# Kernel tuning notes

Hardware: AMD Instinct MI355X
Metric: run time of the kernel (lower is better)

The kernel has to match this reference:

```python
import jax, jax.numpy as jnp
import numpy as np

N_NODES = 50000
N_EDGES = 800000
N_RELS = 65
D = 64
N_GRAPHS = 512


def setup_inputs() -> dict:
    key = jax.random.key(0)
    ks = jax.random.split(key, 20)
    inp = {
        "node_feats": jax.random.normal(ks[0], (N_NODES, D), dtype=jnp.float32),
        "etypes": jax.random.randint(ks[1], (N_EDGES,), 0, N_RELS),
        "src": jax.random.randint(ks[2], (N_EDGES,), 0, N_NODES),
        "dst": jax.random.randint(ks[3], (N_EDGES,), 0, N_NODES),
        "graph_ids": jnp.sort(jax.random.randint(ks[4], (N_NODES,), 0, N_GRAPHS)),
    }
    s = 1.0 / np.sqrt(D)
    # 3 RGCN layers: per-relation weights (basis with num_bases=num_rels == full) + bias
    for i, k in zip(range(1, 4), (ks[5], ks[6], ks[7])):
        inp[f"W_rel{i}"] = jax.random.normal(k, (N_RELS, D, D), dtype=jnp.float32) * s
        inp[f"b{i}"] = jnp.zeros((D,), dtype=jnp.float32)
    # 3 FC layers
    for i, k in zip(range(1, 4), (ks[8], ks[9], ks[10])):
        inp[f"fc_W{i}"] = jax.random.normal(k, (D, D), dtype=jnp.float32) * s
        inp[f"fc_b{i}"] = jnp.zeros((D,), dtype=jnp.float32)
    inp["pred_W"] = jax.random.normal(ks[11], (D, 2), dtype=jnp.float32) * s
    inp["pred_b"] = jnp.zeros((2,), dtype=jnp.float32)
    return inp


def _rgcn_layer(h, W, b, etypes, src, dst):
    # all-relation projection: [N, R, K]
    proj = jnp.einsum('nd,rdk->nrk', h, W)
    # per-edge gather of relation-specific message: [E, K]
    msg = proj[src, etypes]
    # scatter-sum into destination nodes
    agg = jax.ops.segment_sum(msg, dst, num_segments=h.shape[0])
    return jax.nn.relu(agg + b)


def reference(node_feats, etypes, src, dst, graph_ids,
              W_rel1, b1, W_rel2, b2, W_rel3, b3,
              fc_W1, fc_b1, fc_W2, fc_b2, fc_W3, fc_b3,
              pred_W, pred_b):
    h = node_feats
    h = _rgcn_layer(h, W_rel1, b1, etypes, src, dst)
    h = _rgcn_layer(h, W_rel2, b2, etypes, src, dst)
    h = _rgcn_layer(h, W_rel3, b3, etypes, src, dst)
    # sum-pool nodes per graph: [G, D]
    g = jax.ops.segment_sum(h, graph_ids, num_segments=N_GRAPHS)
    g = jax.nn.relu(g @ fc_W1 + fc_b1)
    g = jax.nn.relu(g @ fc_W2 + fc_b2)
    g = jax.nn.relu(g @ fc_W3 + fc_b3)
    return g @ pred_W + pred_b
```

## Files before the change

kernel.cpp:

```cpp
#include <hip/hip_runtime.h>
#include <hip/hip_bf16.h>

#define N_NODES 50000
#define N_EDGES 800000
#define N_RELS 65
#define DIM 64
#define N_GRAPHS 512

#define SORT_BLOCKS 256
#define CHUNK ((N_EDGES + SORT_BLOCKS - 1) / SORT_BLOCKS)

#define SCAN_BLK 512
#define NSCAN_BLKS ((N_NODES + SCAN_BLK - 1) / SCAN_BLK)

#define MSG_BLOCKS 1024
#define NWAVES (MSG_BLOCKS * 4)

typedef __attribute__((ext_vector_type(8))) short short8;
typedef __attribute__((ext_vector_type(4))) float f32x4;


__global__ void conv_h_zero_kernel(const float* __restrict__ x, __hip_bfloat16* __restrict__ y,
                                   int* __restrict__ cnt_d, int* __restrict__ cnt_g) {
    int i = blockIdx.x * 256 + threadIdx.x;
    if (i < N_NODES * DIM) y[i] = __float2bfloat16(x[i]);
    if (i < N_NODES) cnt_d[i] = 0;
    if (i < N_GRAPHS) cnt_g[i] = 0;
}

__global__ void conv_wt3_kernel(const float* __restrict__ W1, const float* __restrict__ W2,
                                const float* __restrict__ W3,
                                __hip_bfloat16* __restrict__ Wt1,
                                __hip_bfloat16* __restrict__ Wt2,
                                __hip_bfloat16* __restrict__ Wt3) {
    const int n = N_RELS * DIM * DIM;
    int i = blockIdx.x * 256 + threadIdx.x;
    if (i >= 3 * n) return;
    int which = i / n, j = i - which * n;
    const float* W = (which == 0) ? W1 : (which == 1) ? W2 : W3;
    __hip_bfloat16* Wt = (which == 0) ? Wt1 : (which == 1) ? Wt2 : Wt3;
    int r = j >> 12, rest = j & 4095;
    int nn = rest >> 6, k = rest & 63;
    Wt[(size_t)r * 4096 + nn * 64 + k] = __float2bfloat16(W[(size_t)r * 4096 + k * 64 + nn]);
}


__global__ __launch_bounds__(256) void hist2_kernel(const int* __restrict__ et,
                                                    int* __restrict__ blk_hist) {
    __shared__ int lh[N_RELS];
    int t = threadIdx.x, b = blockIdx.x;
    if (t < N_RELS) lh[t] = 0;
    __syncthreads();
    int lo = b * CHUNK;
    int hi = lo + CHUNK; if (hi > N_EDGES) hi = N_EDGES;
    for (int i = lo + t; i < hi; i += 256) atomicAdd(&lh[et[i]], 1);
    __syncthreads();
    if (t < N_RELS) blk_hist[b * N_RELS + t] = lh[t];
}

__global__ __launch_bounds__(256) void relwave_kernel(const int* __restrict__ blk_hist,
                                                      int* __restrict__ blk_off,
                                                      int* __restrict__ rel_tot) {
    int wave = blockIdx.x * 4 + (threadIdx.x >> 6);
    int lane = threadIdx.x & 63;
    if (wave >= N_RELS) return;
    int run = 0;
    for (int c = 0; c < SORT_BLOCKS; c += 64) {
        int b = c + lane;
        int v = blk_hist[b * N_RELS + wave];
        int x = v;
        #pragma unroll
        for (int off = 1; off < 64; off <<= 1) {
            int y = __shfl_up(x, off);
            if (lane >= off) x += y;
        }
        blk_off[b * N_RELS + wave] = run + x - v;
        run += __shfl(x, 63);
    }
    if (lane == 0) rel_tot[wave] = run;
}

__global__ __launch_bounds__(128) void relbase_kernel(const int* __restrict__ rel_tot,
                                                      int* __restrict__ rel_ptr,
                                                      int* __restrict__ tile_base) {
    __shared__ int tot[N_RELS];
    int t = threadIdx.x;
    if (t < N_RELS) tot[t] = rel_tot[t];
    __syncthreads();
    if (t == 0) {
        int s = 0, tt = 0;
        for (int q = 0; q < N_RELS; ++q) {
            rel_ptr[q] = s; s += tot[q];
            tile_base[q] = tt; tt += (tot[q] + 15) >> 4;
        }
        rel_ptr[N_RELS] = N_EDGES;
        tile_base[N_RELS] = tt;
    }
}

__global__ __launch_bounds__(256) void scatter2_kernel(
    const int* __restrict__ et, const int* __restrict__ src,
    const int* __restrict__ dst, const int* __restrict__ blk_off,
    const int* __restrict__ rel_ptr,
    int* __restrict__ src_s, int* __restrict__ dst_s) {
    __shared__ int cur[N_RELS];
    int t = threadIdx.x, b = blockIdx.x;
    if (t < N_RELS) cur[t] = blk_off[b * N_RELS + t] + rel_ptr[t];
    __syncthreads();
    int lo = b * CHUNK;
    int hi = lo + CHUNK; if (hi > N_EDGES) hi = N_EDGES;
    for (int i = lo + t; i < hi; i += 256) {
        int r = et[i];
        int p = atomicAdd(&cur[r], 1);
        src_s[p] = src[i];
        dst_s[p] = dst[i];
    }
}


__global__ void histdst_kernel(const int* __restrict__ dst, int* __restrict__ cnt_d) {
    int i = blockIdx.x * 256 + threadIdx.x;
    if (i < N_EDGES) atomicAdd(&cnt_d[dst[i]], 1);
}

__global__ __launch_bounds__(SCAN_BLK) void scanblk_kernel(const int* __restrict__ cnt,
                                                           int* __restrict__ outv,
                                                           int* __restrict__ blk_tot) {
    __shared__ int tmp[SCAN_BLK];
    int t = threadIdx.x;
    int i = blockIdx.x * SCAN_BLK + t;
    int v = (i < N_NODES) ? cnt[i] : 0;
    tmp[t] = v;
    __syncthreads();
    for (int off = 1; off < SCAN_BLK; off <<= 1) {
        int add = (t >= off) ? tmp[t - off] : 0;
        __syncthreads();
        tmp[t] += add;
        __syncthreads();
    }
    if (i < N_NODES) outv[i] = tmp[t] - v;
    if (t == SCAN_BLK - 1) blk_tot[blockIdx.x] = tmp[t];
}

__global__ void scantop_kernel(int* __restrict__ blk_tot, int* __restrict__ blk_base) {
    if (threadIdx.x == 0 && blockIdx.x == 0) {
        int run = 0;
        for (int b = 0; b < NSCAN_BLKS; ++b) { blk_base[b] = run; run += blk_tot[b]; }
    }
}

__global__ __launch_bounds__(SCAN_BLK) void scanadd_kernel(int* __restrict__ outv,
                                                           int* __restrict__ cursor,
                                                           const int* __restrict__ blk_base) {
    int i = blockIdx.x * SCAN_BLK + threadIdx.x;
    if (i < N_NODES) {
        int v = outv[i] + blk_base[blockIdx.x];
        outv[i] = v;
        cursor[i] = v;
    }
}

__global__ void dpos_kernel(const int* __restrict__ dst_s, int* __restrict__ cursor,
                            int* __restrict__ dpos) {
    int i = blockIdx.x * 256 + threadIdx.x;
    if (i < N_EDGES) dpos[i] = atomicAdd(&cursor[dst_s[i]], 1);
}


__global__ void histgid_kernel(const int* __restrict__ gid, int* __restrict__ cnt_g) {
    int i = blockIdx.x * 256 + threadIdx.x;
    if (i < N_NODES) atomicAdd(&cnt_g[gid[i]], 1);
}

__global__ __launch_bounds__(512) void scangid_kernel(const int* __restrict__ cnt_g,
                                                      int* __restrict__ g_ptr) {
    __shared__ int tmp[512];
    int t = threadIdx.x;
    int v = (t < N_GRAPHS) ? cnt_g[t] : 0;
    tmp[t] = v;
    __syncthreads();
    for (int off = 1; off < 512; off <<= 1) {
        int add = (t >= off) ? tmp[t - off] : 0;
        __syncthreads();
        tmp[t] += add;
        __syncthreads();
    }
    if (t < N_GRAPHS) g_ptr[t] = tmp[t] - v;
}


__global__ __launch_bounds__(256) void msg_mfma_kernel(
    const __hip_bfloat16* __restrict__ hb, const __hip_bfloat16* __restrict__ Wt,
    const int* __restrict__ rel_ptr, const int* __restrict__ tile_base,
    const int* __restrict__ src_s, const int* __restrict__ dpos,
    __hip_bfloat16* __restrict__ msg) {
    __shared__ __align__(16) unsigned short stA[4][16 * 72];
    __shared__ __align__(16) float stC[4][16 * 68];

    int t = threadIdx.x;
    int w = t >> 6, lane = t & 63;
    int quad = lane >> 4, m16 = lane & 15;
    int wave = blockIdx.x * 4 + w;

    int ntiles = tile_base[N_RELS];
    int tpw = (ntiles + NWAVES - 1) / NWAVES;
    int T = wave * tpw;
    int T1 = T + tpw; if (T1 > ntiles) T1 = ntiles;
    if (T >= T1) return;

    unsigned short* sa = &stA[w][0];
    float* sc = &stC[w][0];

    int r = 0;
    while (T >= tile_base[r + 1]) ++r;

    while (T < T1) {
        int chunk_end = tile_base[r + 1]; if (chunk_end > T1) chunk_end = T1;
        int e_base = rel_ptr[r], t_base = tile_base[r];
        int seg_end = rel_ptr[r + 1];

        const __hip_bfloat16* Wr = Wt + (size_t)r * (DIM * DIM);
        short8 bf00 = *(const short8*)(Wr + (0 * 16 + m16) * DIM + 0 * 32 + quad * 8);
        short8 bf01 = *(const short8*)(Wr + (1 * 16 + m16) * DIM + 0 * 32 + quad * 8);
        short8 bf02 = *(const short8*)(Wr + (2 * 16 + m16) * DIM + 0 * 32 + quad * 8);
        short8 bf03 = *(const short8*)(Wr + (3 * 16 + m16) * DIM + 0 * 32 + quad * 8);
        short8 bf10 = *(const short8*)(Wr + (0 * 16 + m16) * DIM + 1 * 32 + quad * 8);
        short8 bf11 = *(const short8*)(Wr + (1 * 16 + m16) * DIM + 1 * 32 + quad * 8);
        short8 bf12 = *(const short8*)(Wr + (2 * 16 + m16) * DIM + 1 * 32 + quad * 8);
        short8 bf13 = *(const short8*)(Wr + (3 * 16 + m16) * DIM + 1 * 32 + quad * 8);

        auto eidx = [&](int TT) {
            int i = e_base + (TT - t_base) * 16 + lane;
            return i < N_EDGES ? i : N_EDGES - 1;
        };

        int sv_c, dp_c, sv_n = 0, dp_n = 0, sv_nn = 0, dp_nn = 0;
        uint4 g0_c, g1_c;
        {
            int i0 = eidx(T);
            sv_c = src_s[i0]; dp_c = dpos[i0];
            int r0 = lane >> 3;
            int s0 = __shfl(sv_c, r0);
            int s1 = __shfl(sv_c, r0 + 8);
            g0_c = *(const uint4*)(hb + (size_t)s0 * DIM + (lane & 7) * 8);
            g1_c = *(const uint4*)(hb + (size_t)s1 * DIM + (lane & 7) * 8);
            if (T + 1 < chunk_end) {
                int i1 = eidx(T + 1);
                sv_n = src_s[i1]; dp_n = dpos[i1];
            }
        }

        for (; T < chunk_end; ++T) {
            int e0 = e_base + (T - t_base) * 16;
            int rows = seg_end - e0; if (rows > 16) rows = 16;

            int r0 = lane >> 3;
            *(uint4*)&sa[r0 * 72 + (lane & 7) * 8] = g0_c;
            *(uint4*)&sa[(r0 + 8) * 72 + (lane & 7) * 8] = g1_c;

            uint4 g0_n, g1_n;
            bool hasN = (T + 1 < chunk_end);
            if (hasN) {
                int s0 = __shfl(sv_n, r0);
                int s1 = __shfl(sv_n, r0 + 8);
                g0_n = *(const uint4*)(hb + (size_t)s0 * DIM + (lane & 7) * 8);
                g1_n = *(const uint4*)(hb + (size_t)s1 * DIM + (lane & 7) * 8);
            }
            if (T + 2 < chunk_end) {
                int i2 = eidx(T + 2);
                sv_nn = src_s[i2]; dp_nn = dpos[i2];
            }

            short8 a0 = *(const short8*)&sa[m16 * 72 + quad * 8];
            short8 a1 = *(const short8*)&sa[m16 * 72 + 32 + quad * 8];

            f32x4 c0 = {0.f, 0.f, 0.f, 0.f}, c1 = c0, c2 = c0, c3 = c0;
            c0 = __builtin_amdgcn_mfma_f32_16x16x32_bf16(a0, bf00, c0, 0, 0, 0);
            c1 = __builtin_amdgcn_mfma_f32_16x16x32_bf16(a0, bf01, c1, 0, 0, 0);
            c2 = __builtin_amdgcn_mfma_f32_16x16x32_bf16(a0, bf02, c2, 0, 0, 0);
            c3 = __builtin_amdgcn_mfma_f32_16x16x32_bf16(a0, bf03, c3, 0, 0, 0);
            c0 = __builtin_amdgcn_mfma_f32_16x16x32_bf16(a1, bf10, c0, 0, 0, 0);
            c1 = __builtin_amdgcn_mfma_f32_16x16x32_bf16(a1, bf11, c1, 0, 0, 0);
            c2 = __builtin_amdgcn_mfma_f32_16x16x32_bf16(a1, bf12, c2, 0, 0, 0);
            c3 = __builtin_amdgcn_mfma_f32_16x16x32_bf16(a1, bf13, c3, 0, 0, 0);

            #pragma unroll
            for (int reg = 0; reg < 4; ++reg) {
                int rr = (quad * 4 + reg) * 68 + m16;
                sc[rr +  0] = c0[reg];
                sc[rr + 16] = c1[reg];
                sc[rr + 32] = c2[reg];
                sc[rr + 48] = c3[reg];
            }

            int orow = lane >> 2;
            if (orow < rows) {
                int c0i = (lane & 3) * 16;
                float vs[16];
                *(f32x4*)&vs[0]  = *(const f32x4*)&sc[orow * 68 + c0i + 0];
                *(f32x4*)&vs[4]  = *(const f32x4*)&sc[orow * 68 + c0i + 4];
                *(f32x4*)&vs[8]  = *(const f32x4*)&sc[orow * 68 + c0i + 8];
                *(f32x4*)&vs[12] = *(const f32x4*)&sc[orow * 68 + c0i + 12];
                unsigned short us[16];
                #pragma unroll
                for (int i = 0; i < 16; ++i)
                    us[i] = __hip_bfloat16_raw(__float2bfloat16(vs[i])).x;
                int dprow = __shfl(dp_c, orow);
                __hip_bfloat16* dst = msg + (size_t)dprow * DIM + c0i;
                *(uint4*)dst = *(const uint4*)&us[0];
                *(uint4*)(dst + 8) = *(const uint4*)&us[8];
            }

            if (hasN) { g0_c = g0_n; g1_c = g1_n; }
            sv_c = sv_n; dp_c = dp_n;
            sv_n = sv_nn; dp_n = dp_nn;
        }
        ++r;
        while (T < T1 && T >= tile_base[r + 1]) ++r;
    }
}


__global__ __launch_bounds__(256) void agg_kernel(
    const __hip_bfloat16* __restrict__ msg, const int* __restrict__ row_ptr,
    const int* __restrict__ cnt_d, const float* __restrict__ b,
    __hip_bfloat16* __restrict__ hout) {
    int wave = blockIdx.x * 4 + (threadIdx.x >> 6);
    int lane = threadIdx.x & 63;
    if (wave >= N_NODES) return;
    int j0 = row_ptr[wave];
    int n  = cnt_d[wave];
    int rgrp = lane >> 3, dgrp = lane & 7;

    float a[8] = {0.f, 0.f, 0.f, 0.f, 0.f, 0.f, 0.f, 0.f};
    for (int jj = 0; jj < n; jj += 8) {
        int row = jj + rgrp;
        if (row < n) {
            uint4 d = *(const uint4*)(msg + (size_t)(j0 + row) * DIM + dgrp * 8);
            a[0] += __uint_as_float(d.x << 16);
            a[1] += __uint_as_float(d.x & 0xffff0000u);
            a[2] += __uint_as_float(d.y << 16);
            a[3] += __uint_as_float(d.y & 0xffff0000u);
            a[4] += __uint_as_float(d.z << 16);
            a[5] += __uint_as_float(d.z & 0xffff0000u);
            a[6] += __uint_as_float(d.w << 16);
            a[7] += __uint_as_float(d.w & 0xffff0000u);
        }
    }
    #pragma unroll
    for (int i = 0; i < 8; ++i) {
        a[i] += __shfl_xor(a[i], 8);
        a[i] += __shfl_xor(a[i], 16);
        a[i] += __shfl_xor(a[i], 32);
    }
    if (rgrp == 0) {
        unsigned short us[8];
        #pragma unroll
        for (int i = 0; i < 8; ++i) {
            float v = a[i] + b[dgrp * 8 + i];
            us[i] = __hip_bfloat16_raw(__float2bfloat16(v > 0.f ? v : 0.f)).x;
        }
        *(uint4*)(hout + (size_t)wave * DIM + dgrp * 8) = *(const uint4*)us;
    }
}


__global__ __launch_bounds__(256) void poolfc_kernel(
    const __hip_bfloat16* __restrict__ h, const int* __restrict__ g_ptr,
    const int* __restrict__ cnt_g,
    const float* __restrict__ W1, const float* __restrict__ b1,
    const float* __restrict__ W2, const float* __restrict__ b2,
    const float* __restrict__ W3, const float* __restrict__ b3,
    const float* __restrict__ pW, const float* __restrict__ pb,
    float* __restrict__ out) {
    int wave = blockIdx.x * 4 + (threadIdx.x >> 6);
    int lane = threadIdx.x & 63;
    if (wave >= N_GRAPHS) return;
    int j0 = g_ptr[wave];
    int n  = cnt_g[wave];
    int rgrp = lane >> 3, dgrp = lane & 7;

    float a[8] = {0.f, 0.f, 0.f, 0.f, 0.f, 0.f, 0.f, 0.f};
    for (int jj = 0; jj < n; jj += 8) {
        int row = jj + rgrp;
        if (row < n) {
            uint4 d = *(const uint4*)(h + (size_t)(j0 + row) * DIM + dgrp * 8);
            a[0] += __uint_as_float(d.x << 16);
            a[1] += __uint_as_float(d.x & 0xffff0000u);
            a[2] += __uint_as_float(d.y << 16);
            a[3] += __uint_as_float(d.y & 0xffff0000u);
            a[4] += __uint_as_float(d.z << 16);
            a[5] += __uint_as_float(d.z & 0xffff0000u);
            a[6] += __uint_as_float(d.w << 16);
            a[7] += __uint_as_float(d.w & 0xffff0000u);
        }
    }
    #pragma unroll
    for (int i = 0; i < 8; ++i) {
        a[i] += __shfl_xor(a[i], 8);
        a[i] += __shfl_xor(a[i], 16);
        a[i] += __shfl_xor(a[i], 32);
    }
    float v;
    {
        float acc = b1[lane];
        #pragma unroll
        for (int o = 0; o < 8; ++o)
            #pragma unroll
            for (int q = 0; q < 8; ++q)
                acc += __shfl(a[o], q) * W1[(q * 8 + o) * DIM + lane];
        v = acc > 0.f ? acc : 0.f;
    }
    {
        float acc = b2[lane];
        #pragma unroll
        for (int d = 0; d < DIM; ++d)
            acc += __shfl(v, d) * W2[d * DIM + lane];
        v = acc > 0.f ? acc : 0.f;
    }
    {
        float acc = b3[lane];
        #pragma unroll
        for (int d = 0; d < DIM; ++d)
            acc += __shfl(v, d) * W3[d * DIM + lane];
        v = acc > 0.f ? acc : 0.f;
    }
    float p0 = v * pW[lane * 2 + 0];
    float p1 = v * pW[lane * 2 + 1];
    #pragma unroll
    for (int off = 32; off > 0; off >>= 1) {
        p0 += __shfl_down(p0, off);
        p1 += __shfl_down(p1, off);
    }
    if (lane == 0) {
        out[wave * 2 + 0] = p0 + pb[0];
        out[wave * 2 + 1] = p1 + pb[1];
    }
}


extern "C" void kernel_launch(void* const* d_in, const int* in_sizes, int n_in,
                              void* d_out, int out_size, void* d_ws, size_t ws_size,
                              hipStream_t stream) {
    const float* node_feats = (const float*)d_in[0];
    const int*   etypes     = (const int*)d_in[1];
    const int*   src        = (const int*)d_in[2];
    const int*   dst        = (const int*)d_in[3];
    const int*   graph_ids  = (const int*)d_in[4];
    const float* W1 = (const float*)d_in[5];
    const float* b1 = (const float*)d_in[6];
    const float* W2 = (const float*)d_in[7];
    const float* b2 = (const float*)d_in[8];
    const float* W3 = (const float*)d_in[9];
    const float* b3 = (const float*)d_in[10];
    const float* fcW1 = (const float*)d_in[11];
    const float* fcb1 = (const float*)d_in[12];
    const float* fcW2 = (const float*)d_in[13];
    const float* fcb2 = (const float*)d_in[14];
    const float* fcW3 = (const float*)d_in[15];
    const float* fcb3 = (const float*)d_in[16];
    const float* pW = (const float*)d_in[17];
    const float* pb = (const float*)d_in[18];
    float* out = (float*)d_out;

    char* p = (char*)d_ws;
    auto alloc = [&](size_t bytes) -> void* {
        void* r = (void*)p;
        p += (bytes + 255) & ~(size_t)255;
        return r;
    };
    int* blk_hist  = (int*)alloc((size_t)SORT_BLOCKS * N_RELS * sizeof(int));
    int* blk_off   = (int*)alloc((size_t)SORT_BLOCKS * N_RELS * sizeof(int));
    int* rel_tot   = (int*)alloc(N_RELS * sizeof(int));
    int* rel_ptr   = (int*)alloc((N_RELS + 1) * sizeof(int));
    int* tile_base = (int*)alloc((N_RELS + 1) * sizeof(int));
    int* src_s     = (int*)alloc((size_t)N_EDGES * sizeof(int));
    int* dst_s     = (int*)alloc((size_t)N_EDGES * sizeof(int));
    int* dpos      = (int*)alloc((size_t)N_EDGES * sizeof(int));
    int* cnt_d     = (int*)alloc((size_t)N_NODES * sizeof(int));
    int* row_ptr   = (int*)alloc((size_t)N_NODES * sizeof(int));
    int* cursor_d  = (int*)alloc((size_t)N_NODES * sizeof(int));
    int* blk_tot   = (int*)alloc(NSCAN_BLKS * sizeof(int));
    int* blk_base  = (int*)alloc(NSCAN_BLKS * sizeof(int));
    int* cnt_g     = (int*)alloc(N_GRAPHS * sizeof(int));
    int* g_ptr     = (int*)alloc(N_GRAPHS * sizeof(int));
    __hip_bfloat16* hb0 = (__hip_bfloat16*)alloc((size_t)N_NODES * DIM * sizeof(__hip_bfloat16));
    __hip_bfloat16* hb1 = (__hip_bfloat16*)alloc((size_t)N_NODES * DIM * sizeof(__hip_bfloat16));
    __hip_bfloat16* Wt1 = (__hip_bfloat16*)alloc((size_t)N_RELS * DIM * DIM * sizeof(__hip_bfloat16));
    __hip_bfloat16* Wt2 = (__hip_bfloat16*)alloc((size_t)N_RELS * DIM * DIM * sizeof(__hip_bfloat16));
    __hip_bfloat16* Wt3 = (__hip_bfloat16*)alloc((size_t)N_RELS * DIM * DIM * sizeof(__hip_bfloat16));
    __hip_bfloat16* msg = (__hip_bfloat16*)alloc((size_t)N_EDGES * DIM * sizeof(__hip_bfloat16));

    const int EBLK = (N_EDGES + 255) / 256;
    const int HBLK = (N_NODES * DIM + 255) / 256;
    const int W3BLK = (3 * N_RELS * DIM * DIM + 255) / 256;
    const int NBLK256 = (N_NODES + 255) / 256;
    const int AGG_BLOCKS = (N_NODES + 3) / 4;

    conv_h_zero_kernel<<<HBLK, 256, 0, stream>>>(node_feats, hb0, cnt_d, cnt_g);
    conv_wt3_kernel<<<W3BLK, 256, 0, stream>>>(W1, W2, W3, Wt1, Wt2, Wt3);

    hist2_kernel<<<SORT_BLOCKS, 256, 0, stream>>>(etypes, blk_hist);
    relwave_kernel<<<(N_RELS + 3) / 4, 256, 0, stream>>>(blk_hist, blk_off, rel_tot);
    relbase_kernel<<<1, 128, 0, stream>>>(rel_tot, rel_ptr, tile_base);
    scatter2_kernel<<<SORT_BLOCKS, 256, 0, stream>>>(etypes, src, dst, blk_off, rel_ptr,
                                                     src_s, dst_s);

    histdst_kernel<<<EBLK, 256, 0, stream>>>(dst, cnt_d);
    scanblk_kernel<<<NSCAN_BLKS, SCAN_BLK, 0, stream>>>(cnt_d, row_ptr, blk_tot);
    scantop_kernel<<<1, 64, 0, stream>>>(blk_tot, blk_base);
    scanadd_kernel<<<NSCAN_BLKS, SCAN_BLK, 0, stream>>>(row_ptr, cursor_d, blk_base);
    dpos_kernel<<<EBLK, 256, 0, stream>>>(dst_s, cursor_d, dpos);

    histgid_kernel<<<NBLK256, 256, 0, stream>>>(graph_ids, cnt_g);
    scangid_kernel<<<1, 512, 0, stream>>>(cnt_g, g_ptr);

    msg_mfma_kernel<<<MSG_BLOCKS, 256, 0, stream>>>(hb0, Wt1, rel_ptr, tile_base,
                                                    src_s, dpos, msg);
    agg_kernel<<<AGG_BLOCKS, 256, 0, stream>>>(msg, row_ptr, cnt_d, b1, hb1);

    msg_mfma_kernel<<<MSG_BLOCKS, 256, 0, stream>>>(hb1, Wt2, rel_ptr, tile_base,
                                                    src_s, dpos, msg);
    agg_kernel<<<AGG_BLOCKS, 256, 0, stream>>>(msg, row_ptr, cnt_d, b2, hb0);

    msg_mfma_kernel<<<MSG_BLOCKS, 256, 0, stream>>>(hb0, Wt3, rel_ptr, tile_base,
                                                    src_s, dpos, msg);
    agg_kernel<<<AGG_BLOCKS, 256, 0, stream>>>(msg, row_ptr, cnt_d, b3, hb1);

    poolfc_kernel<<<(N_GRAPHS + 3) / 4, 256, 0, stream>>>(hb1, g_ptr, cnt_g,
                                                          fcW1, fcb1, fcW2, fcb2,
                                                          fcW3, fcb3, pW, pb, out);
}
```

Before: 421.4 us.

## Fuse preprocessing, message, aggregation and pooling into a cooperative persistent kernel

Merges the dst and graph-id histograms and the weight transpose into the relation histogram kernel, and merges the two relation-offset kernels into one. The scans, dpos computation, three message/aggregate layers and the pool+FC head now run in a single cooperative mega-kernel separated by grid.sync() barriers. The goal is to remove the launch overhead and idle gaps of roughly twenty small kernels. In exchange, grid-wide barriers are added and the grid size is capped by occupancy, which may limit parallelism in the heavy message and aggregation phases.

```diff
diff --git a/kernel.cpp b/kernel.cpp
--- a/kernel.cpp
+++ b/kernel.cpp
@@ -1,5 +1,8 @@
 #include <hip/hip_runtime.h>
 #include <hip/hip_bf16.h>
+#include <hip/hip_cooperative_groups.h>
+
+namespace cg = cooperative_groups;
 
 #define N_NODES 50000
 #define N_EDGES 800000
@@ -10,11 +13,10 @@
 #define SORT_BLOCKS 256
 #define CHUNK ((N_EDGES + SORT_BLOCKS - 1) / SORT_BLOCKS)
 
-#define SCAN_BLK 512
+#define SCAN_BLK 256
 #define NSCAN_BLKS ((N_NODES + SCAN_BLK - 1) / SCAN_BLK)
 
-#define MSG_BLOCKS 1024
-#define NWAVES (MSG_BLOCKS * 4)
+#define MAX_MEGA_BLOCKS 1024
 
 typedef __attribute__((ext_vector_type(8))) short short8;
 typedef __attribute__((ext_vector_type(4))) float f32x4;
@@ -28,64 +30,66 @@
     if (i < N_GRAPHS) cnt_g[i] = 0;
 }
 
-__global__ void conv_wt3_kernel(const float* __restrict__ W1, const float* __restrict__ W2,
-                                const float* __restrict__ W3,
-                                __hip_bfloat16* __restrict__ Wt1,
-                                __hip_bfloat16* __restrict__ Wt2,
-                                __hip_bfloat16* __restrict__ Wt3) {
-    const int n = N_RELS * DIM * DIM;
-    int i = blockIdx.x * 256 + threadIdx.x;
-    if (i >= 3 * n) return;
-    int which = i / n, j = i - which * n;
-    const float* W = (which == 0) ? W1 : (which == 1) ? W2 : W3;
-    __hip_bfloat16* Wt = (which == 0) ? Wt1 : (which == 1) ? Wt2 : Wt3;
-    int r = j >> 12, rest = j & 4095;
-    int nn = rest >> 6, k = rest & 63;
-    Wt[(size_t)r * 4096 + nn * 64 + k] = __float2bfloat16(W[(size_t)r * 4096 + k * 64 + nn]);
-}
-
-
-__global__ __launch_bounds__(256) void hist2_kernel(const int* __restrict__ et,
-                                                    int* __restrict__ blk_hist) {
+
+__global__ __launch_bounds__(256) void hist_all_kernel(
+    const int* __restrict__ et, const int* __restrict__ dst,
+    const int* __restrict__ gid, int* __restrict__ blk_hist,
+    int* __restrict__ cnt_d, int* __restrict__ cnt_g,
+    const float* __restrict__ W1, const float* __restrict__ W2,
+    const float* __restrict__ W3,
+    __hip_bfloat16* __restrict__ Wt1, __hip_bfloat16* __restrict__ Wt2,
+    __hip_bfloat16* __restrict__ Wt3) {
     __shared__ int lh[N_RELS];
     int t = threadIdx.x, b = blockIdx.x;
+    int gtid = b * 256 + t;
     if (t < N_RELS) lh[t] = 0;
     __syncthreads();
     int lo = b * CHUNK;
     int hi = lo + CHUNK; if (hi > N_EDGES) hi = N_EDGES;
-    for (int i = lo + t; i < hi; i += 256) atomicAdd(&lh[et[i]], 1);
+    for (int i = lo + t; i < hi; i += 256) {
+        atomicAdd(&lh[et[i]], 1);
+        atomicAdd(&cnt_d[dst[i]], 1);
+    }
+    for (int i = gtid; i < N_NODES; i += SORT_BLOCKS * 256)
+        atomicAdd(&cnt_g[gid[i]], 1);
+    const int WN = N_RELS * DIM * DIM;
+    for (int i = gtid; i < 3 * WN; i += SORT_BLOCKS * 256) {
+        int which = i / WN, j = i - which * WN;
+        const float* W = (which == 0) ? W1 : (which == 1) ? W2 : W3;
+        __hip_bfloat16* Wt = (which == 0) ? Wt1 : (which == 1) ? Wt2 : Wt3;
+        int r = j >> 12, rest = j & 4095;
+        int nn = rest >> 6, k = rest & 63;
+        Wt[(size_t)r * 4096 + nn * 64 + k] =
+            __float2bfloat16(W[(size_t)r * 4096 + k * 64 + nn]);
+    }
     __syncthreads();
     if (t < N_RELS) blk_hist[b * N_RELS + t] = lh[t];
 }
 
-__global__ __launch_bounds__(256) void relwave_kernel(const int* __restrict__ blk_hist,
-                                                      int* __restrict__ blk_off,
-                                                      int* __restrict__ rel_tot) {
-    int wave = blockIdx.x * 4 + (threadIdx.x >> 6);
-    int lane = threadIdx.x & 63;
-    if (wave >= N_RELS) return;
-    int run = 0;
-    for (int c = 0; c < SORT_BLOCKS; c += 64) {
-        int b = c + lane;
-        int v = blk_hist[b * N_RELS + wave];
-        int x = v;
-        #pragma unroll
-        for (int off = 1; off < 64; off <<= 1) {
-            int y = __shfl_up(x, off);
-            if (lane >= off) x += y;
-        }
-        blk_off[b * N_RELS + wave] = run + x - v;
-        run += __shfl(x, 63);
-    }
-    if (lane == 0) rel_tot[wave] = run;
-}
-
-__global__ __launch_bounds__(128) void relbase_kernel(const int* __restrict__ rel_tot,
-                                                      int* __restrict__ rel_ptr,
-                                                      int* __restrict__ tile_base) {
+
+__global__ __launch_bounds__(1024) void relwave2_kernel(const int* __restrict__ blk_hist,
+                                                        int* __restrict__ blk_off,
+                                                        int* __restrict__ rel_ptr,
+                                                        int* __restrict__ tile_base) {
     __shared__ int tot[N_RELS];
     int t = threadIdx.x;
-    if (t < N_RELS) tot[t] = rel_tot[t];
+    int w = t >> 6, lane = t & 63;
+    for (int r = w; r < N_RELS; r += 16) {
+        int run = 0;
+        for (int c = 0; c < SORT_BLOCKS; c += 64) {
+            int b = c + lane;
+            int v = blk_hist[b * N_RELS + r];
+            int x = v;
+            #pragma unroll
+            for (int off = 1; off < 64; off <<= 1) {
+                int y = __shfl_up(x, off);
+                if (lane >= off) x += y;
+            }
+            blk_off[b * N_RELS + r] = run + x - v;
+            run += __shfl(x, 63);
+        }
+        if (lane == 0) tot[r] = run;
+    }
     __syncthreads();
     if (t == 0) {
         int s = 0, tt = 0;
@@ -97,6 +101,7 @@
         tile_base[N_RELS] = tt;
     }
 }
+
 
 __global__ __launch_bounds__(256) void scatter2_kernel(
     const int* __restrict__ et, const int* __restrict__ src,
@@ -118,323 +123,305 @@
 }
 
 
-__global__ void histdst_kernel(const int* __restrict__ dst, int* __restrict__ cnt_d) {
-    int i = blockIdx.x * 256 + threadIdx.x;
-    if (i < N_EDGES) atomicAdd(&cnt_d[dst[i]], 1);
-}
-
-__global__ __launch_bounds__(SCAN_BLK) void scanblk_kernel(const int* __restrict__ cnt,
-                                                           int* __restrict__ outv,
-                                                           int* __restrict__ blk_tot) {
-    __shared__ int tmp[SCAN_BLK];
-    int t = threadIdx.x;
-    int i = blockIdx.x * SCAN_BLK + t;
-    int v = (i < N_NODES) ? cnt[i] : 0;
-    tmp[t] = v;
-    __syncthreads();
-    for (int off = 1; off < SCAN_BLK; off <<= 1) {
-        int add = (t >= off) ? tmp[t - off] : 0;
-        __syncthreads();
-        tmp[t] += add;
-        __syncthreads();
-    }
-    if (i < N_NODES) outv[i] = tmp[t] - v;
-    if (t == SCAN_BLK - 1) blk_tot[blockIdx.x] = tmp[t];
-}
-
-__global__ void scantop_kernel(int* __restrict__ blk_tot, int* __restrict__ blk_base) {
-    if (threadIdx.x == 0 && blockIdx.x == 0) {
-        int run = 0;
-        for (int b = 0; b < NSCAN_BLKS; ++b) { blk_base[b] = run; run += blk_tot[b]; }
-    }
-}
-
-__global__ __launch_bounds__(SCAN_BLK) void scanadd_kernel(int* __restrict__ outv,
-                                                           int* __restrict__ cursor,
-                                                           const int* __restrict__ blk_base) {
-    int i = blockIdx.x * SCAN_BLK + threadIdx.x;
-    if (i < N_NODES) {
-        int v = outv[i] + blk_base[blockIdx.x];
-        outv[i] = v;
-        cursor[i] = v;
-    }
-}
-
-__global__ void dpos_kernel(const int* __restrict__ dst_s, int* __restrict__ cursor,
-                            int* __restrict__ dpos) {
-    int i = blockIdx.x * 256 + threadIdx.x;
-    if (i < N_EDGES) dpos[i] = atomicAdd(&cursor[dst_s[i]], 1);
-}
-
-
-__global__ void histgid_kernel(const int* __restrict__ gid, int* __restrict__ cnt_g) {
-    int i = blockIdx.x * 256 + threadIdx.x;
-    if (i < N_NODES) atomicAdd(&cnt_g[gid[i]], 1);
-}
-
-__global__ __launch_bounds__(512) void scangid_kernel(const int* __restrict__ cnt_g,
-                                                      int* __restrict__ g_ptr) {
-    __shared__ int tmp[512];
-    int t = threadIdx.x;
-    int v = (t < N_GRAPHS) ? cnt_g[t] : 0;
-    tmp[t] = v;
-    __syncthreads();
-    for (int off = 1; off < 512; off <<= 1) {
-        int add = (t >= off) ? tmp[t - off] : 0;
-        __syncthreads();
-        tmp[t] += add;
-        __syncthreads();
-    }
-    if (t < N_GRAPHS) g_ptr[t] = tmp[t] - v;
-}
-
-
-__global__ __launch_bounds__(256) void msg_mfma_kernel(
-    const __hip_bfloat16* __restrict__ hb, const __hip_bfloat16* __restrict__ Wt,
-    const int* __restrict__ rel_ptr, const int* __restrict__ tile_base,
-    const int* __restrict__ src_s, const int* __restrict__ dpos,
-    __hip_bfloat16* __restrict__ msg) {
+struct MegaParams {
+    __hip_bfloat16 *hb0, *hb1;
+    const __hip_bfloat16 *Wt1, *Wt2, *Wt3;
+    const float *b1, *b2, *b3;
+    const int *rel_ptr, *tile_base, *src_s, *dst_s;
+    int *dpos, *cnt_d, *row_ptr, *cursor, *blk_tot, *blk_base;
+    const int *cnt_g; int *g_ptr;
+    __hip_bfloat16 *msg;
+    const float *fcW1, *fcb1, *fcW2, *fcb2, *fcW3, *fcb3, *pW, *pb;
+    float *out;
+};
+
+__global__ __launch_bounds__(256, 2) void mega_kernel(MegaParams P) {
+    cg::grid_group grid = cg::this_grid();
     __shared__ __align__(16) unsigned short stA[4][16 * 72];
     __shared__ __align__(16) float stC[4][16 * 68];
-
-    int t = threadIdx.x;
+    __shared__ int s_tmp[SCAN_BLK];
+
+    int t = threadIdx.x, b = blockIdx.x;
     int w = t >> 6, lane = t & 63;
     int quad = lane >> 4, m16 = lane & 15;
-    int wave = blockIdx.x * 4 + w;
-
-    int ntiles = tile_base[N_RELS];
-    int tpw = (ntiles + NWAVES - 1) / NWAVES;
-    int T = wave * tpw;
-    int T1 = T + tpw; if (T1 > ntiles) T1 = ntiles;
-    if (T >= T1) return;
+    int wave = b * 4 + w;
+    int gtid = b * 256 + t;
+    int nwaves = gridDim.x * 4;
+    int nthreads = gridDim.x * 256;
+
+    if (b < NSCAN_BLKS) {
+        int i = b * SCAN_BLK + t;
+        int v = (i < N_NODES) ? P.cnt_d[i] : 0;
+        s_tmp[t] = v;
+        __syncthreads();
+        for (int off = 1; off < SCAN_BLK; off <<= 1) {
+            int add = (t >= off) ? s_tmp[t - off] : 0;
+            __syncthreads();
+            s_tmp[t] += add;
+            __syncthreads();
+        }
+        if (i < N_NODES) P.row_ptr[i] = s_tmp[t] - v;
+        if (t == SCAN_BLK - 1) P.blk_tot[b] = s_tmp[t];
+    }
+    grid.sync();
+
+    if (b == 0 && t == 0) {
+        int run = 0;
+        for (int c = 0; c < NSCAN_BLKS; ++c) { P.blk_base[c] = run; run += P.blk_tot[c]; }
+    }
+    if (b == 1 && w == 0) {
+        int run = 0;
+        for (int c = 0; c < N_GRAPHS; c += 64) {
+            int v = P.cnt_g[c + lane];
+            int x = v;
+            #pragma unroll
+            for (int off = 1; off < 64; off <<= 1) {
+                int y = __shfl_up(x, off);
+                if (lane >= off) x += y;
+            }
+            P.g_ptr[c + lane] = run + x - v;
+            run += __shfl(x, 63);
+        }
+    }
+    grid.sync();
+
+    for (int i = gtid; i < N_NODES; i += nthreads) {
+        int v = P.row_ptr[i] + P.blk_base[i >> 8];
+        P.row_ptr[i] = v;
+        P.cursor[i] = v;
+    }
+    grid.sync();
+
+    for (int i = gtid; i < N_EDGES; i += nthreads)
+        P.dpos[i] = atomicAdd(&P.cursor[P.dst_s[i]], 1);
+    grid.sync();
 
     unsigned short* sa = &stA[w][0];
     float* sc = &stC[w][0];
-
-    int r = 0;
-    while (T >= tile_base[r + 1]) ++r;
-
-    while (T < T1) {
-        int chunk_end = tile_base[r + 1]; if (chunk_end > T1) chunk_end = T1;
-        int e_base = rel_ptr[r], t_base = tile_base[r];
-        int seg_end = rel_ptr[r + 1];
-
-        const __hip_bfloat16* Wr = Wt + (size_t)r * (DIM * DIM);
-        short8 bf00 = *(const short8*)(Wr + (0 * 16 + m16) * DIM + 0 * 32 + quad * 8);
-        short8 bf01 = *(const short8*)(Wr + (1 * 16 + m16) * DIM + 0 * 32 + quad * 8);
-        short8 bf02 = *(const short8*)(Wr + (2 * 16 + m16) * DIM + 0 * 32 + quad * 8);
-        short8 bf03 = *(const short8*)(Wr + (3 * 16 + m16) * DIM + 0 * 32 + quad * 8);
-        short8 bf10 = *(const short8*)(Wr + (0 * 16 + m16) * DIM + 1 * 32 + quad * 8);
-        short8 bf11 = *(const short8*)(Wr + (1 * 16 + m16) * DIM + 1 * 32 + quad * 8);
-        short8 bf12 = *(const short8*)(Wr + (2 * 16 + m16) * DIM + 1 * 32 + quad * 8);
-        short8 bf13 = *(const short8*)(Wr + (3 * 16 + m16) * DIM + 1 * 32 + quad * 8);
-
-        auto eidx = [&](int TT) {
-            int i = e_base + (TT - t_base) * 16 + lane;
-            return i < N_EDGES ? i : N_EDGES - 1;
-        };
-
-        int sv_c, dp_c, sv_n = 0, dp_n = 0, sv_nn = 0, dp_nn = 0;
-        uint4 g0_c, g1_c;
+    int ntiles = P.tile_base[N_RELS];
+
+    for (int layer = 0; layer < 3; ++layer) {
+        const __hip_bfloat16* hin  = (layer & 1) ? P.hb1 : P.hb0;
+        __hip_bfloat16*       hout = (layer & 1) ? P.hb0 : P.hb1;
+        const __hip_bfloat16* Wt = (layer == 0) ? P.Wt1 : (layer == 1) ? P.Wt2 : P.Wt3;
+        const float* bias = (layer == 0) ? P.b1 : (layer == 1) ? P.b2 : P.b3;
+
         {
-            int i0 = eidx(T);
-            sv_c = src_s[i0]; dp_c = dpos[i0];
-            int r0 = lane >> 3;
-            int s0 = __shfl(sv_c, r0);
-            int s1 = __shfl(sv_c, r0 + 8);
-            g0_c = *(const uint4*)(hb + (size_t)s0 * DIM + (lane & 7) * 8);
-            g1_c = *(const uint4*)(hb + (size_t)s1 * DIM + (lane & 7) * 8);
-            if (T + 1 < chunk_end) {
-                int i1 = eidx(T + 1);
-                sv_n = src_s[i1]; dp_n = dpos[i1];
+            int tpw = (ntiles + nwaves - 1) / nwaves;
+            int T = wave * tpw;
+            int T1 = T + tpw; if (T1 > ntiles) T1 = ntiles;
+            if (T < T1) {
+                int r = 0;
+                while (T >= P.tile_base[r + 1]) ++r;
+                while (T < T1) {
+                    int chunk_end = P.tile_base[r + 1]; if (chunk_end > T1) chunk_end = T1;
+                    int e_base = P.rel_ptr[r], t_base = P.tile_base[r];
+                    int seg_end = P.rel_ptr[r + 1];
+
+                    const __hip_bfloat16* Wr = Wt + (size_t)r * (DIM * DIM);
+                    short8 bf00 = *(const short8*)(Wr + (0 * 16 + m16) * DIM + quad * 8);
+                    short8 bf01 = *(const short8*)(Wr + (1 * 16 + m16) * DIM + quad * 8);
+                    short8 bf02 = *(const short8*)(Wr + (2 * 16 + m16) * DIM + quad * 8);
+                    short8 bf03 = *(const short8*)(Wr + (3 * 16 + m16) * DIM + quad * 8);
+                    short8 bf10 = *(const short8*)(Wr + (0 * 16 + m16) * DIM + 32 + quad * 8);
+                    short8 bf11 = *(const short8*)(Wr + (1 * 16 + m16) * DIM + 32 + quad * 8);
+                    short8 bf12 = *(const short8*)(Wr + (2 * 16 + m16) * DIM + 32 + quad * 8);
+                    short8 bf13 = *(const short8*)(Wr + (3 * 16 + m16) * DIM + 32 + quad * 8);
+
+                    auto eidx = [&](int TT) {
+                        int i = e_base + (TT - t_base) * 16 + lane;
+                        return i < N_EDGES ? i : N_EDGES - 1;
+                    };
+
+                    int sv_c, dp_c, sv_n = 0, dp_n = 0, sv_nn = 0, dp_nn = 0;
+                    uint4 g0_c, g1_c;
+                    {
+                        int i0 = eidx(T);
+                        sv_c = P.src_s[i0]; dp_c = P.dpos[i0];
+                        int r0 = lane >> 3;
+                        int s0 = __shfl(sv_c, r0);
+                        int s1 = __shfl(sv_c, r0 + 8);
+                        g0_c = *(const uint4*)(hin + (size_t)s0 * DIM + (lane & 7) * 8);
+                        g1_c = *(const uint4*)(hin + (size_t)s1 * DIM + (lane & 7) * 8);
+                        if (T + 1 < chunk_end) {
+                            int i1 = eidx(T + 1);
+                            sv_n = P.src_s[i1]; dp_n = P.dpos[i1];
+                        }
+                    }
+
+                    for (; T < chunk_end; ++T) {
+                        int e0 = e_base + (T - t_base) * 16;
+                        int rows = seg_end - e0; if (rows > 16) rows = 16;
+
+                        int r0 = lane >> 3;
+                        *(uint4*)&sa[r0 * 72 + (lane & 7) * 8] = g0_c;
+                        *(uint4*)&sa[(r0 + 8) * 72 + (lane & 7) * 8] = g1_c;
+
+                        uint4 g0_n, g1_n;
+                        bool hasN = (T + 1 < chunk_end);
+                        if (hasN) {
+                            int s0 = __shfl(sv_n, r0);
+                            int s1 = __shfl(sv_n, r0 + 8);
+                            g0_n = *(const uint4*)(hin + (size_t)s0 * DIM + (lane & 7) * 8);
+                            g1_n = *(const uint4*)(hin + (size_t)s1 * DIM + (lane & 7) * 8);
+                        }
+                        if (T + 2 < chunk_end) {
+                            int i2 = eidx(T + 2);
+                            sv_nn = P.src_s[i2]; dp_nn = P.dpos[i2];
+                        }
+
+                        short8 a0 = *(const short8*)&sa[m16 * 72 + quad * 8];
+                        short8 a1 = *(const short8*)&sa[m16 * 72 + 32 + quad * 8];
+
+                        f32x4 c0 = {0.f, 0.f, 0.f, 0.f}, c1 = c0, c2 = c0, c3 = c0;
+                        c0 = __builtin_amdgcn_mfma_f32_16x16x32_bf16(a0, bf00, c0, 0, 0, 0);
+                        c1 = __builtin_amdgcn_mfma_f32_16x16x32_bf16(a0, bf01, c1, 0, 0, 0);
+                        c2 = __builtin_amdgcn_mfma_f32_16x16x32_bf16(a0, bf02, c2, 0, 0, 0);
+                        c3 = __builtin_amdgcn_mfma_f32_16x16x32_bf16(a0, bf03, c3, 0, 0, 0);
+                        c0 = __builtin_amdgcn_mfma_f32_16x16x32_bf16(a1, bf10, c0, 0, 0, 0);
+                        c1 = __builtin_amdgcn_mfma_f32_16x16x32_bf16(a1, bf11, c1, 0, 0, 0);
+                        c2 = __builtin_amdgcn_mfma_f32_16x16x32_bf16(a1, bf12, c2, 0, 0, 0);
+                        c3 = __builtin_amdgcn_mfma_f32_16x16x32_bf16(a1, bf13, c3, 0, 0, 0);
+
+                        #pragma unroll
+                        for (int reg = 0; reg < 4; ++reg) {
+                            int rr = (quad * 4 + reg) * 68 + m16;
+                            sc[rr +  0] = c0[reg];
+                            sc[rr + 16] = c1[reg];
+                            sc[rr + 32] = c2[reg];
+                            sc[rr + 48] = c3[reg];
+                        }
+
+                        int orow = lane >> 2;
+                        if (orow < rows) {
+                            int c0i = (lane & 3) * 16;
+                            float vs[16];
+                            *(f32x4*)&vs[0]  = *(const f32x4*)&sc[orow * 68 + c0i + 0];
+                            *(f32x4*)&vs[4]  = *(const f32x4*)&sc[orow * 68 + c0i + 4];
+                            *(f32x4*)&vs[8]  = *(const f32x4*)&sc[orow * 68 + c0i + 8];
+                            *(f32x4*)&vs[12] = *(const f32x4*)&sc[orow * 68 + c0i + 12];
+                            unsigned short us[16];
+                            #pragma unroll
+                            for (int i = 0; i < 16; ++i)
+                                us[i] = __hip_bfloat16_raw(__float2bfloat16(vs[i])).x;
+                            int dprow = __shfl(dp_c, orow);
+                            __hip_bfloat16* dstp = P.msg + (size_t)dprow * DIM + c0i;
+                            *(uint4*)dstp = *(const uint4*)&us[0];
+                            *(uint4*)(dstp + 8) = *(const uint4*)&us[8];
+                        }
+
+                        if (hasN) { g0_c = g0_n; g1_c = g1_n; }
+                        sv_c = sv_n; dp_c = dp_n;
+                        sv_n = sv_nn; dp_n = dp_nn;
+                    }
+                    ++r;
+                    while (T < T1 && T >= P.tile_base[r + 1]) ++r;
+                }
             }
         }
-
-        for (; T < chunk_end; ++T) {
-            int e0 = e_base + (T - t_base) * 16;
-            int rows = seg_end - e0; if (rows > 16) rows = 16;
-
-            int r0 = lane >> 3;
-            *(uint4*)&sa[r0 * 72 + (lane & 7) * 8] = g0_c;
-            *(uint4*)&sa[(r0 + 8) * 72 + (lane & 7) * 8] = g1_c;
-
-            uint4 g0_n, g1_n;
-            bool hasN = (T + 1 < chunk_end);
-            if (hasN) {
-                int s0 = __shfl(sv_n, r0);
-                int s1 = __shfl(sv_n, r0 + 8);
-                g0_n = *(const uint4*)(hb + (size_t)s0 * DIM + (lane & 7) * 8);
-                g1_n = *(const uint4*)(hb + (size_t)s1 * DIM + (lane & 7) * 8);
+        grid.sync();
+
+        {
+            int rgrp = lane >> 3, dgrp = lane & 7;
+            for (int node = wave; node < N_NODES; node += nwaves) {
+                int j0 = P.row_ptr[node];
+                int n  = P.cnt_d[node];
+                float a[8] = {0.f, 0.f, 0.f, 0.f, 0.f, 0.f, 0.f, 0.f};
+                for (int jj = 0; jj < n; jj += 8) {
+                    int row = jj + rgrp;
+                    if (row < n) {
+                        uint4 d = *(const uint4*)(P.msg + (size_t)(j0 + row) * DIM + dgrp * 8);
+                        a[0] += __uint_as_float(d.x << 16);
+                        a[1] += __uint_as_float(d.x & 0xffff0000u);
+                        a[2] += __uint_as_float(d.y << 16);
+                        a[3] += __uint_as_float(d.y & 0xffff0000u);
+                        a[4] += __uint_as_float(d.z << 16);
+                        a[5] += __uint_as_float(d.z & 0xffff0000u);
+                        a[6] += __uint_as_float(d.w << 16);
+                        a[7] += __uint_as_float(d.w & 0xffff0000u);
+                    }
+                }
+                #pragma unroll
+                for (int i = 0; i < 8; ++i) {
+                    a[i] += __shfl_xor(a[i], 8);
+                    a[i] += __shfl_xor(a[i], 16);
+                    a[i] += __shfl_xor(a[i], 32);
+                }
+                if (rgrp == 0) {
+                    unsigned short us[8];
+                    #pragma unroll
+                    for (int i = 0; i < 8; ++i) {
+                        float v = a[i] + bias[dgrp * 8 + i];
+                        us[i] = __hip_bfloat16_raw(__float2bfloat16(v > 0.f ? v : 0.f)).x;
+                    }
+                    *(uint4*)(hout + (size_t)node * DIM + dgrp * 8) = *(const uint4*)us;
+                }
             }
-            if (T + 2 < chunk_end) {
-                int i2 = eidx(T + 2);
-                sv_nn = src_s[i2]; dp_nn = dpos[i2];
+        }
+        grid.sync();
+    }
+
+    if (wave < N_GRAPHS) {
+        const __hip_bfloat16* h = P.hb1;
+        int j0 = P.g_ptr[wave];
+        int n  = P.cnt_g[wave];
+        int rgrp = lane >> 3, dgrp = lane & 7;
+        float a[8] = {0.f, 0.f, 0.f, 0.f, 0.f, 0.f, 0.f, 0.f};
+        for (int jj = 0; jj < n; jj += 8) {
+            int row = jj + rgrp;
+            if (row < n) {
+                uint4 d = *(const uint4*)(h + (size_t)(j0 + row) * DIM + dgrp * 8);
+                a[0] += __uint_as_float(d.x << 16);
+                a[1] += __uint_as_float(d.x & 0xffff0000u);
+                a[2] += __uint_as_float(d.y << 16);
+                a[3] += __uint_as_float(d.y & 0xffff0000u);
+                a[4] += __uint_as_float(d.z << 16);
+                a[5] += __uint_as_float(d.z & 0xffff0000u);
+                a[6] += __uint_as_float(d.w << 16);
+                a[7] += __uint_as_float(d.w & 0xffff0000u);
             }
-
-            short8 a0 = *(const short8*)&sa[m16 * 72 + quad * 8];
-            short8 a1 = *(const short8*)&sa[m16 * 72 + 32 + quad * 8];
-
-            f32x4 c0 = {0.f, 0.f, 0.f, 0.f}, c1 = c0, c2 = c0, c3 = c0;
-            c0 = __builtin_amdgcn_mfma_f32_16x16x32_bf16(a0, bf00, c0, 0, 0, 0);
-            c1 = __builtin_amdgcn_mfma_f32_16x16x32_bf16(a0, bf01, c1, 0, 0, 0);
-            c2 = __builtin_amdgcn_mfma_f32_16x16x32_bf16(a0, bf02, c2, 0, 0, 0);
-            c3 = __builtin_amdgcn_mfma_f32_16x16x32_bf16(a0, bf03, c3, 0, 0, 0);
-            c0 = __builtin_amdgcn_mfma_f32_16x16x32_bf16(a1, bf10, c0, 0, 0, 0);
-            c1 = __builtin_amdgcn_mfma_f32_16x16x32_bf16(a1, bf11, c1, 0, 0, 0);
-            c2 = __builtin_amdgcn_mfma_f32_16x16x32_bf16(a1, bf12, c2, 0, 0, 0);
-            c3 = __builtin_amdgcn_mfma_f32_16x16x32_bf16(a1, bf13, c3, 0, 0, 0);
-
-            #pragma unroll
-            for (int reg = 0; reg < 4; ++reg) {
-                int rr = (quad * 4 + reg) * 68 + m16;
-                sc[rr +  0] = c0[reg];
-                sc[rr + 16] = c1[reg];
-                sc[rr + 32] = c2[reg];
-                sc[rr + 48] = c3[reg];
-            }
-
-            int orow = lane >> 2;
-            if (orow < rows) {
-                int c0i = (lane & 3) * 16;
-                float vs[16];
-                *(f32x4*)&vs[0]  = *(const f32x4*)&sc[orow * 68 + c0i + 0];
-                *(f32x4*)&vs[4]  = *(const f32x4*)&sc[orow * 68 + c0i + 4];
-                *(f32x4*)&vs[8]  = *(const f32x4*)&sc[orow * 68 + c0i + 8];
-                *(f32x4*)&vs[12] = *(const f32x4*)&sc[orow * 68 + c0i + 12];
-                unsigned short us[16];
-                #pragma unroll
-                for (int i = 0; i < 16; ++i)
-                    us[i] = __hip_bfloat16_raw(__float2bfloat16(vs[i])).x;
-                int dprow = __shfl(dp_c, orow);
-                __hip_bfloat16* dst = msg + (size_t)dprow * DIM + c0i;
-                *(uint4*)dst = *(const uint4*)&us[0];
-                *(uint4*)(dst + 8) = *(const uint4*)&us[8];
-            }
-
-            if (hasN) { g0_c = g0_n; g1_c = g1_n; }
-            sv_c = sv_n; dp_c = dp_n;
-            sv_n = sv_nn; dp_n = dp_nn;
-        }
-        ++r;
-        while (T < T1 && T >= tile_base[r + 1]) ++r;
-    }
-}
-
-
-__global__ __launch_bounds__(256) void agg_kernel(
-    const __hip_bfloat16* __restrict__ msg, const int* __restrict__ row_ptr,
-    const int* __restrict__ cnt_d, const float* __restrict__ b,
-    __hip_bfloat16* __restrict__ hout) {
-    int wave = blockIdx.x * 4 + (threadIdx.x >> 6);
-    int lane = threadIdx.x & 63;
-    if (wave >= N_NODES) return;
-    int j0 = row_ptr[wave];
-    int n  = cnt_d[wave];
-    int rgrp = lane >> 3, dgrp = lane & 7;
-
-    float a[8] = {0.f, 0.f, 0.f, 0.f, 0.f, 0.f, 0.f, 0.f};
-    for (int jj = 0; jj < n; jj += 8) {
-        int row = jj + rgrp;
-        if (row < n) {
-            uint4 d = *(const uint4*)(msg + (size_t)(j0 + row) * DIM + dgrp * 8);
-            a[0] += __uint_as_float(d.x << 16);
-            a[1] += __uint_as_float(d.x & 0xffff0000u);
-            a[2] += __uint_as_float(d.y << 16);
-            a[3] += __uint_as_float(d.y & 0xffff0000u);
-            a[4] += __uint_as_float(d.z << 16);
-            a[5] += __uint_as_float(d.z & 0xffff0000u);
-            a[6] += __uint_as_float(d.w << 16);
-            a[7] += __uint_as_float(d.w & 0xffff0000u);
-        }
-    }
-    #pragma unroll
-    for (int i = 0; i < 8; ++i) {
-        a[i] += __shfl_xor(a[i], 8);
-        a[i] += __shfl_xor(a[i], 16);
-        a[i] += __shfl_xor(a[i], 32);
-    }
-    if (rgrp == 0) {
-        unsigned short us[8];
+        }
         #pragma unroll
         for (int i = 0; i < 8; ++i) {
-            float v = a[i] + b[dgrp * 8 + i];
-            us[i] = __hip_bfloat16_raw(__float2bfloat16(v > 0.f ? v : 0.f)).x;
-        }
-        *(uint4*)(hout + (size_t)wave * DIM + dgrp * 8) = *(const uint4*)us;
-    }
-}
-
-
-__global__ __launch_bounds__(256) void poolfc_kernel(
-    const __hip_bfloat16* __restrict__ h, const int* __restrict__ g_ptr,
-    const int* __restrict__ cnt_g,
-    const float* __restrict__ W1, const float* __restrict__ b1,
-    const float* __restrict__ W2, const float* __restrict__ b2,
-    const float* __restrict__ W3, const float* __restrict__ b3,
-    const float* __restrict__ pW, const float* __restrict__ pb,
-    float* __restrict__ out) {
-    int wave = blockIdx.x * 4 + (threadIdx.x >> 6);
-    int lane = threadIdx.x & 63;
-    if (wave >= N_GRAPHS) return;
-    int j0 = g_ptr[wave];
-    int n  = cnt_g[wave];
-    int rgrp = lane >> 3, dgrp = lane & 7;
-
-    float a[8] = {0.f, 0.f, 0.f, 0.f, 0.f, 0.f, 0.f, 0.f};
-    for (int jj = 0; jj < n; jj += 8) {
-        int row = jj + rgrp;
-        if (row < n) {
-            uint4 d = *(const uint4*)(h + (size_t)(j0 + row) * DIM + dgrp * 8);
-            a[0] += __uint_as_float(d.x << 16);
-            a[1] += __uint_as_float(d.x & 0xffff0000u);
-            a[2] += __uint_as_float(d.y << 16);
-            a[3] += __uint_as_float(d.y & 0xffff0000u);
-            a[4] += __uint_as_float(d.z << 16);
-            a[5] += __uint_as_float(d.z & 0xffff0000u);
-            a[6] += __uint_as_float(d.w << 16);
-            a[7] += __uint_as_float(d.w & 0xffff0000u);
-        }
-    }
-    #pragma unroll
-    for (int i = 0; i < 8; ++i) {
-        a[i] += __shfl_xor(a[i], 8);
-        a[i] += __shfl_xor(a[i], 16);
-        a[i] += __shfl_xor(a[i], 32);
-    }
-    float v;
-    {
-        float acc = b1[lane];
+            a[i] += __shfl_xor(a[i], 8);
+            a[i] += __shfl_xor(a[i], 16);
+            a[i] += __shfl_xor(a[i], 32);
+        }
+        float v;
+        {
+            float acc = P.fcb1[lane];
+            #pragma unroll
+            for (int o = 0; o < 8; ++o)
+                #pragma unroll
+                for (int q = 0; q < 8; ++q)
+                    acc += __shfl(a[o], q) * P.fcW1[(q * 8 + o) * DIM + lane];
+            v = acc > 0.f ? acc : 0.f;
+        }
+        {
+            float acc = P.fcb2[lane];
+            #pragma unroll
+            for (int d = 0; d < DIM; ++d)
+                acc += __shfl(v, d) * P.fcW2[d * DIM + lane];
+            v = acc > 0.f ? acc : 0.f;
+        }
+        {
+            float acc = P.fcb3[lane];
+            #pragma unroll
+            for (int d = 0; d < DIM; ++d)
+                acc += __shfl(v, d) * P.fcW3[d * DIM + lane];
+            v = acc > 0.f ? acc : 0.f;
+        }
+        float p0 = v * P.pW[lane * 2 + 0];
+        float p1 = v * P.pW[lane * 2 + 1];
         #pragma unroll
-        for (int o = 0; o < 8; ++o)
-            #pragma unroll
-            for (int q = 0; q < 8; ++q)
-                acc += __shfl(a[o], q) * W1[(q * 8 + o) * DIM + lane];
-        v = acc > 0.f ? acc : 0.f;
-    }
-    {
-        float acc = b2[lane];
-        #pragma unroll
-        for (int d = 0; d < DIM; ++d)
-            acc += __shfl(v, d) * W2[d * DIM + lane];
-        v = acc > 0.f ? acc : 0.f;
-    }
-    {
-        float acc = b3[lane];
-        #pragma unroll
-        for (int d = 0; d < DIM; ++d)
-            acc += __shfl(v, d) * W3[d * DIM + lane];
-        v = acc > 0.f ? acc : 0.f;
-    }
-    float p0 = v * pW[lane * 2 + 0];
-    float p1 = v * pW[lane * 2 + 1];
-    #pragma unroll
-    for (int off = 32; off > 0; off >>= 1) {
-        p0 += __shfl_down(p0, off);
-        p1 += __shfl_down(p1, off);
-    }
-    if (lane == 0) {
-        out[wave * 2 + 0] = p0 + pb[0];
-        out[wave * 2 + 1] = p1 + pb[1];
+        for (int off = 32; off > 0; off >>= 1) {
+            p0 += __shfl_down(p0, off);
+            p1 += __shfl_down(p1, off);
+        }
+        if (lane == 0) {
+            P.out[wave * 2 + 0] = p0 + P.pb[0];
+            P.out[wave * 2 + 1] = p1 + P.pb[1];
+        }
     }
 }
 
@@ -471,7 +458,6 @@
     };
     int* blk_hist  = (int*)alloc((size_t)SORT_BLOCKS * N_RELS * sizeof(int));
     int* blk_off   = (int*)alloc((size_t)SORT_BLOCKS * N_RELS * sizeof(int));
-    int* rel_tot   = (int*)alloc(N_RELS * sizeof(int));
     int* rel_ptr   = (int*)alloc((N_RELS + 1) * sizeof(int));
     int* tile_base = (int*)alloc((N_RELS + 1) * sizeof(int));
     int* src_s     = (int*)alloc((size_t)N_EDGES * sizeof(int));
@@ -491,43 +477,38 @@
     __hip_bfloat16* Wt3 = (__hip_bfloat16*)alloc((size_t)N_RELS * DIM * DIM * sizeof(__hip_bfloat16));
     __hip_bfloat16* msg = (__hip_bfloat16*)alloc((size_t)N_EDGES * DIM * sizeof(__hip_bfloat16));
 
-    const int EBLK = (N_EDGES + 255) / 256;
     const int HBLK = (N_NODES * DIM + 255) / 256;
-    const int W3BLK = (3 * N_RELS * DIM * DIM + 255) / 256;
-    const int NBLK256 = (N_NODES + 255) / 256;
-    const int AGG_BLOCKS = (N_NODES + 3) / 4;
 
     conv_h_zero_kernel<<<HBLK, 256, 0, stream>>>(node_feats, hb0, cnt_d, cnt_g);
-    conv_wt3_kernel<<<W3BLK, 256, 0, stream>>>(W1, W2, W3, Wt1, Wt2, Wt3);
-
-    hist2_kernel<<<SORT_BLOCKS, 256, 0, stream>>>(etypes, blk_hist);
-    relwave_kernel<<<(N_RELS + 3) / 4, 256, 0, stream>>>(blk_hist, blk_off, rel_tot);
-    relbase_kernel<<<1, 128, 0, stream>>>(rel_tot, rel_ptr, tile_base);
+    hist_all_kernel<<<SORT_BLOCKS, 256, 0, stream>>>(etypes, dst, graph_ids, blk_hist,
+                                                     cnt_d, cnt_g, W1, W2, W3,
+                                                     Wt1, Wt2, Wt3);
+    relwave2_kernel<<<1, 1024, 0, stream>>>(blk_hist, blk_off, rel_ptr, tile_base);
     scatter2_kernel<<<SORT_BLOCKS, 256, 0, stream>>>(etypes, src, dst, blk_off, rel_ptr,
                                                      src_s, dst_s);
 
-    histdst_kernel<<<EBLK, 256, 0, stream>>>(dst, cnt_d);
-    scanblk_kernel<<<NSCAN_BLKS, SCAN_BLK, 0, stream>>>(cnt_d, row_ptr, blk_tot);
-    scantop_kernel<<<1, 64, 0, stream>>>(blk_tot, blk_base);
-    scanadd_kernel<<<NSCAN_BLKS, SCAN_BLK, 0, stream>>>(row_ptr, cursor_d, blk_base);
-    dpos_kernel<<<EBLK, 256, 0, stream>>>(dst_s, cursor_d, dpos);
-
-    histgid_kernel<<<NBLK256, 256, 0, stream>>>(graph_ids, cnt_g);
-    scangid_kernel<<<1, 512, 0, stream>>>(cnt_g, g_ptr);
-
-    msg_mfma_kernel<<<MSG_BLOCKS, 256, 0, stream>>>(hb0, Wt1, rel_ptr, tile_base,
-                                                    src_s, dpos, msg);
-    agg_kernel<<<AGG_BLOCKS, 256, 0, stream>>>(msg, row_ptr, cnt_d, b1, hb1);
-
-    msg_mfma_kernel<<<MSG_BLOCKS, 256, 0, stream>>>(hb1, Wt2, rel_ptr, tile_base,
-                                                    src_s, dpos, msg);
-    agg_kernel<<<AGG_BLOCKS, 256, 0, stream>>>(msg, row_ptr, cnt_d, b2, hb0);
-
-    msg_mfma_kernel<<<MSG_BLOCKS, 256, 0, stream>>>(hb0, Wt3, rel_ptr, tile_base,
-                                                    src_s, dpos, msg);
-    agg_kernel<<<AGG_BLOCKS, 256, 0, stream>>>(msg, row_ptr, cnt_d, b3, hb1);
-
-    poolfc_kernel<<<(N_GRAPHS + 3) / 4, 256, 0, stream>>>(hb1, g_ptr, cnt_g,
-                                                          fcW1, fcb1, fcW2, fcb2,
-                                                          fcW3, fcb3, pW, pb, out);
+    MegaParams P;
+    P.hb0 = hb0; P.hb1 = hb1;
+    P.Wt1 = Wt1; P.Wt2 = Wt2; P.Wt3 = Wt3;
+    P.b1 = b1; P.b2 = b2; P.b3 = b3;
+    P.rel_ptr = rel_ptr; P.tile_base = tile_base; P.src_s = src_s; P.dst_s = dst_s;
+    P.dpos = dpos; P.cnt_d = cnt_d; P.row_ptr = row_ptr; P.cursor = cursor_d;
+    P.blk_tot = blk_tot; P.blk_base = blk_base;
+    P.cnt_g = cnt_g; P.g_ptr = g_ptr;
+    P.msg = msg;
+    P.fcW1 = fcW1; P.fcb1 = fcb1; P.fcW2 = fcW2; P.fcb2 = fcb2;
+    P.fcW3 = fcW3; P.fcb3 = fcb3; P.pW = pW; P.pb = pb;
+    P.out = out;
+
+    int blkPerCU = 0;
+    (void)hipOccupancyMaxActiveBlocksPerMultiprocessor(&blkPerCU,
+                                                       (const void*)mega_kernel, 256, 0);
+    if (blkPerCU < 1) blkPerCU = 1;
+    int grid = blkPerCU * 256;
+    if (grid > MAX_MEGA_BLOCKS) grid = MAX_MEGA_BLOCKS;
+    if (grid < 256) grid = 256;
+
+    void* args[] = { &P };
+    hipLaunchCooperativeKernel((const void*)mega_kernel, dim3(grid), dim3(256),
+                               args, 0, stream);
 }
```

Result: slower. 1.131 ms (+168.4%).
